# Performance work log

Hardware: AMD Instinct MI355X
Metric: run time of the kernel (lower is better)

## Reference

```python
import jax, jax.numpy as jnp
import numpy as np

# Conv config matching init_kwargs
C_IN, C_OUT = 128, 256
KH, KW = 3, 3
STRIDE = (1, 1)
PADDING = ((1, 1), (1, 1))
DILATION = (1, 1)
B, H, W = 32, 56, 56


def setup_inputs() -> dict:
    key = jax.random.key(0)
    k1, k2, k3 = jax.random.split(key, 3)
    x = jax.random.normal(k1, (B, C_IN, H, W), dtype=jnp.float32)
    # Flattened weight as stored by Conv2DUF: conv.weight.view(O,-1).t() -> [C*kh*kw, O]
    weight = jax.random.normal(k2, (C_IN * KH * KW, C_OUT), dtype=jnp.float32) * 0.02
    bias = jax.random.normal(k3, (C_OUT,), dtype=jnp.float32) * 0.02
    return {"x": x, "weight": weight, "bias": bias}


def reference(x, weight, bias):
    # Conv2DUF computes unfold(x) @ weight + bias, which is exactly a 2D
    # cross-correlation with the original conv kernel. Recover the [O,C,kh,kw]
    # kernel from the flattened [C*kh*kw, O] matrix and use the fused conv
    # primitive (same math, no giant im2col buffer).
    kernel = weight.T.reshape(C_OUT, C_IN, KH, KW)
    out = jax.lax.conv_general_dilated(
        x, kernel,
        window_strides=STRIDE,
        padding=PADDING,
        rhs_dilation=DILATION,
        dimension_numbers=("NCHW", "OIHW", "NCHW"),
    )
    return out + bias[None, :, None, None]
```

## Files before the change

### kernel.cpp

```cpp
#include <hip/hip_runtime.h>
#include <stdint.h>


#define C_INQ 128
#define C_OUTQ 256
#define HDIM 56
#define WDIM 56
#define BDIM 32
#define HP 58
#define WP 58
#define HWPIX (HDIM * WDIM)
#define XT_ELEMS ((size_t)BDIM * HP * WP * C_INQ)
#define XT_BYTES (XT_ELEMS * 2)

typedef __bf16 bf16x8 __attribute__((ext_vector_type(8)));
typedef unsigned short ushort8 __attribute__((ext_vector_type(8)));
typedef float floatx4 __attribute__((ext_vector_type(4)));

__device__ __forceinline__ unsigned short f2bf(float f) {
  union { float f; unsigned int u; } v; v.f = f;
  unsigned int u = v.u;
  unsigned int r = u + 0x7FFFu + ((u >> 16) & 1u);
  return (unsigned short)(r >> 16);
}

__global__ __launch_bounds__(256) void pad_transpose_kernel(
    const float* __restrict__ x, unsigned short* __restrict__ xt) {
  const int blk = blockIdx.x;
  const int b = blk / HP;
  const int hp = blk % HP;
  const int t = threadIdx.x;
  unsigned short* __restrict__ xtrow = xt + (size_t)(b * HP + hp) * (WP * C_INQ);
  if (hp == 0 || hp == HP - 1) {
    for (int i = t; i < WP * C_INQ; i += 256) xtrow[i] = 0;
    return;
  }
  __shared__ float lds[C_INQ * 57];
  const int h = hp - 1;
  const float* __restrict__ xb = x + (size_t)b * C_INQ * HWPIX + h * WDIM;
  for (int i = t; i < C_INQ * WDIM; i += 256) {
    int c = i / WDIM, w = i % WDIM;
    lds[c * 57 + w] = xb[(size_t)c * HWPIX + w];
  }
  __syncthreads();
  for (int i = t; i < WP * C_INQ; i += 256) {
    int wp = i >> 7, c = i & 127;
    float v = (wp == 0 || wp == WP - 1) ? 0.0f : lds[c * 57 + (wp - 1)];
    xtrow[i] = f2bf(v);
  }
}

__global__ __launch_bounds__(256) void weight_transform_kernel(
    const float* __restrict__ w, unsigned short* __restrict__ wt) {
  int idx = blockIdx.x * 256 + threadIdx.x;
  int khw = idx >> 15;
  int r = idx & 32767;
  int n = r >> 7;
  int c = r & 127;
  wt[idx] = f2bf(w[(size_t)(c * 9 + khw) * C_OUTQ + n]);
}

#define BM 128
#define BN 128
#define BK 32

__global__ __launch_bounds__(256, 2) void conv_gemm_kernel(
    const unsigned short* __restrict__ xt,
    const unsigned short* __restrict__ wt,
    const float* __restrict__ bias,
    float* __restrict__ out) {
  __shared__ __align__(16) unsigned short ldsA[BM * BK];
  __shared__ __align__(16) unsigned short ldsB[BN * BK];

  const int t = threadIdx.x;
  const int lane = t & 63;
  const int wave = t >> 6;
  const int tile_m = blockIdx.x;
  const int tile_n = blockIdx.y;
  const int n0 = tile_n * BN;

  size_t baseA[2], baseB[2];
#pragma unroll
  for (int r = 0; r < 2; ++r) {
    int j = r * 256 + t;
    int pix = tile_m * BM + (j >> 2);
    int b = pix / HWPIX;
    int p = pix - b * HWPIX;
    int h = p / WDIM;
    int w = p - h * WDIM;
    baseA[r] = (size_t)((b * HP + h) * WP + w) * C_INQ + (j & 3) * 8;
    baseB[r] = (size_t)(n0 + (j >> 2)) * C_INQ + (j & 3) * 8;
  }
  unsigned short* ldsA_dst[2] = { ldsA + wave * 512, ldsA + 2048 + wave * 512 };
  unsigned short* ldsB_dst[2] = { ldsB + wave * 512, ldsB + 2048 + wave * 512 };

  const int wm = (wave >> 1) * 64;
  const int wn = (wave & 1) * 64;
  const int mrow = lane & 15;
  const int quad = lane >> 4;
  int aoff[4], boff[4];
#pragma unroll
  for (int i = 0; i < 4; ++i) {
    aoff[i] = (wm + i * 16 + mrow) * BK + quad * 8;
    boff[i] = (wn + i * 16 + mrow) * BK + quad * 8;
  }

  floatx4 acc[4][4] = {};

  for (int s = 0; s < 36; ++s) {
    const int khw = s >> 2;
    const int c0 = (s & 3) * 32;
    const int kh = khw / 3;
    const int kw = khw - kh * 3;
    const size_t koffA = (size_t)(kh * WP + kw) * C_INQ + c0;
    const size_t koffB = (size_t)khw * (C_OUTQ * C_INQ) + c0;
#pragma unroll
    for (int r = 0; r < 2; ++r) {
      __builtin_amdgcn_global_load_lds(
          (const __attribute__((address_space(1))) unsigned int*)(xt + baseA[r] + koffA),
          (__attribute__((address_space(3))) unsigned int*)ldsA_dst[r], 16, 0, 0);
      __builtin_amdgcn_global_load_lds(
          (const __attribute__((address_space(1))) unsigned int*)(wt + baseB[r] + koffB),
          (__attribute__((address_space(3))) unsigned int*)ldsB_dst[r], 16, 0, 0);
    }
    __syncthreads();

    bf16x8 afr[4], bfr[4];
#pragma unroll
    for (int i = 0; i < 4; ++i)
      afr[i] = __builtin_bit_cast(bf16x8, *(const ushort8*)(ldsA + aoff[i]));
#pragma unroll
    for (int i = 0; i < 4; ++i)
      bfr[i] = __builtin_bit_cast(bf16x8, *(const ushort8*)(ldsB + boff[i]));
#pragma unroll
    for (int i = 0; i < 4; ++i)
#pragma unroll
      for (int jn = 0; jn < 4; ++jn)
        acc[i][jn] = __builtin_amdgcn_mfma_f32_16x16x32_bf16(afr[i], bfr[jn], acc[i][jn], 0, 0, 0);

    __syncthreads();
  }

#pragma unroll
  for (int jn = 0; jn < 4; ++jn) {
    const int ng = n0 + wn + jn * 16 + mrow;
    const float bv = bias[ng];
#pragma unroll
    for (int i = 0; i < 4; ++i) {
      const int mbase = tile_m * BM + wm + i * 16 + quad * 4;
#pragma unroll
      for (int rg = 0; rg < 4; ++rg) {
        const int mg = mbase + rg;
        const int b = mg / HWPIX;
        const int p = mg - b * HWPIX;
        out[(size_t)b * (C_OUTQ * HWPIX) + (size_t)ng * HWPIX + p] = acc[i][jn][rg] + bv;
      }
    }
  }
}

extern "C" void kernel_launch(void* const* d_in, const int* in_sizes, int n_in,
                              void* d_out, int out_size, void* d_ws, size_t ws_size,
                              hipStream_t stream) {
  const float* x    = (const float*)d_in[0];
  const float* w    = (const float*)d_in[1];
  const float* bias = (const float*)d_in[2];
  float* out = (float*)d_out;

  unsigned short* xt = (unsigned short*)d_ws;
  unsigned short* wt = (unsigned short*)((char*)d_ws + XT_BYTES);

  hipLaunchKernelGGL(pad_transpose_kernel, dim3(BDIM * HP), dim3(256), 0, stream, x, xt);
  hipLaunchKernelGGL(weight_transform_kernel, dim3(1152), dim3(256), 0, stream, w, wt);
  hipLaunchKernelGGL(conv_gemm_kernel, dim3(784, 2), dim3(256), 0, stream, xt, wt, bias, out);
}
```

Baseline: 263.9 us.

## Vectorize pre-transforms, double GEMM K-step with XOR-swizzled LDS, vector stores

The input pad-transpose kernel now reads float4 and writes packed 8-element bf16 vectors. The weight transform now goes through an LDS tile and writes uint4 vectors. The conv GEMM doubles BK to 64, which halves the number of barrier-separated steps, and XOR-swizzles the LDS layout to avoid bank conflicts on fragment reads. The epilogue writes floatx4 along the pixel dimension. Risks are the larger LDS footprint and dropping the min-2-blocks launch bound, both of which may lower occupancy. The floatx4 store also assumes each 4-pixel group never crosses a batch boundary, which holds because HW is divisible by 4.

```diff
diff --git a/kernel.cpp b/kernel.cpp
--- a/kernel.cpp
+++ b/kernel.cpp
@@ -23,6 +23,9 @@
   unsigned int r = u + 0x7FFFu + ((u >> 16) & 1u);
   return (unsigned short)(r >> 16);
 }
+__device__ __forceinline__ unsigned int pack2(float a, float b) {
+  return (unsigned int)f2bf(a) | ((unsigned int)f2bf(b) << 16);
+}
 
 __global__ __launch_bounds__(256) void pad_transpose_kernel(
     const float* __restrict__ x, unsigned short* __restrict__ xt) {
@@ -30,41 +33,72 @@
   const int b = blk / HP;
   const int hp = blk % HP;
   const int t = threadIdx.x;
-  unsigned short* __restrict__ xtrow = xt + (size_t)(b * HP + hp) * (WP * C_INQ);
+  uint4* __restrict__ xtrow4 = (uint4*)(xt + (size_t)(b * HP + hp) * (WP * C_INQ));
   if (hp == 0 || hp == HP - 1) {
-    for (int i = t; i < WP * C_INQ; i += 256) xtrow[i] = 0;
+    for (int i = t; i < 928; i += 256) xtrow4[i] = make_uint4(0, 0, 0, 0);
     return;
   }
-  __shared__ float lds[C_INQ * 57];
+  __shared__ float lds[C_INQ * 62];
   const int h = hp - 1;
-  const float* __restrict__ xb = x + (size_t)b * C_INQ * HWPIX + h * WDIM;
-  for (int i = t; i < C_INQ * WDIM; i += 256) {
-    int c = i / WDIM, w = i % WDIM;
-    lds[c * 57 + w] = xb[(size_t)c * HWPIX + w];
+  const float* __restrict__ xb = x + (size_t)b * C_INQ * HWPIX + (size_t)h * WDIM;
+  for (int i = t; i < 1792; i += 256) {
+    int c = i / 14, w4 = (i - c * 14) * 4;
+    const float4 v = *(const float4*)(xb + (size_t)c * HWPIX + w4);
+    float* d = lds + c * 62 + w4;
+    *(float2*)d = make_float2(v.x, v.y);
+    *(float2*)(d + 2) = make_float2(v.z, v.w);
   }
   __syncthreads();
-  for (int i = t; i < WP * C_INQ; i += 256) {
-    int wp = i >> 7, c = i & 127;
-    float v = (wp == 0 || wp == WP - 1) ? 0.0f : lds[c * 57 + (wp - 1)];
-    xtrow[i] = f2bf(v);
+  for (int j = t; j < 928; j += 256) {
+    int wp = j >> 4, c8 = (j & 15) * 8;
+    uint4 o;
+    if (wp == 0 || wp == WP - 1) {
+      o = make_uint4(0, 0, 0, 0);
+    } else {
+      const float* s = lds + c8 * 62 + (wp - 1);
+      o.x = pack2(s[0],   s[62]);
+      o.y = pack2(s[124], s[186]);
+      o.z = pack2(s[248], s[310]);
+      o.w = pack2(s[372], s[434]);
+    }
+    xtrow4[j] = o;
   }
 }
 
 __global__ __launch_bounds__(256) void weight_transform_kernel(
     const float* __restrict__ w, unsigned short* __restrict__ wt) {
-  int idx = blockIdx.x * 256 + threadIdx.x;
-  int khw = idx >> 15;
-  int r = idx & 32767;
-  int n = r >> 7;
-  int c = r & 127;
-  wt[idx] = f2bf(w[(size_t)(c * 9 + khw) * C_OUTQ + n]);
+  const int bx = blockIdx.x;
+  const int khw = bx >> 4;
+  const int r4 = bx & 15;
+  const int n0w = (r4 >> 2) * 64;
+  const int c32 = (r4 & 3) * 32;
+  const int t = threadIdx.x;
+  __shared__ float lds[32 * 66];
+#pragma unroll
+  for (int r = 0; r < 8; ++r) {
+    int idx = r * 256 + t;
+    int n = idx & 63, c = idx >> 6;
+    lds[c * 66 + n] = w[(size_t)((c32 + c) * 9 + khw) * C_OUTQ + n0w + n];
+  }
+  __syncthreads();
+  {
+    int n = t >> 2, c8 = (t & 3) * 8;
+    const float* s = lds + c8 * 66 + n;
+    uint4 o;
+    o.x = pack2(s[0],   s[66]);
+    o.y = pack2(s[132], s[198]);
+    o.z = pack2(s[264], s[330]);
+    o.w = pack2(s[396], s[462]);
+    *(uint4*)(wt + (size_t)khw * (C_OUTQ * C_INQ) + (size_t)(n0w + n) * C_INQ + c32 + c8) = o;
+  }
 }
 
 #define BM 128
 #define BN 128
-#define BK 32
-
-__global__ __launch_bounds__(256, 2) void conv_gemm_kernel(
+#define BK 64
+#define STEPS 18
+
+__global__ __launch_bounds__(256) void conv_gemm_kernel(
     const unsigned short* __restrict__ xt,
     const unsigned short* __restrict__ wt,
     const float* __restrict__ bias,
@@ -79,82 +113,91 @@
   const int tile_n = blockIdx.y;
   const int n0 = tile_n * BN;
 
-  size_t baseA[2], baseB[2];
-#pragma unroll
-  for (int r = 0; r < 2; ++r) {
-    int j = r * 256 + t;
-    int pix = tile_m * BM + (j >> 2);
+  int gbaseA[4], gbaseB[4];
+#pragma unroll
+  for (int r = 0; r < 4; ++r) {
+    int g = r * 256 + t;
+    int row = g >> 3;
+    int kpart = (g & 7) ^ (row & 7);
+    int pix = tile_m * BM + row;
     int b = pix / HWPIX;
     int p = pix - b * HWPIX;
     int h = p / WDIM;
     int w = p - h * WDIM;
-    baseA[r] = (size_t)((b * HP + h) * WP + w) * C_INQ + (j & 3) * 8;
-    baseB[r] = (size_t)(n0 + (j >> 2)) * C_INQ + (j & 3) * 8;
-  }
-  unsigned short* ldsA_dst[2] = { ldsA + wave * 512, ldsA + 2048 + wave * 512 };
-  unsigned short* ldsB_dst[2] = { ldsB + wave * 512, ldsB + 2048 + wave * 512 };
+    gbaseA[r] = ((b * HP + h) * WP + w) * C_INQ + kpart * 8;
+    gbaseB[r] = (n0 + row) * C_INQ + kpart * 8;
+  }
+  unsigned short* ldsA_dst[4];
+  unsigned short* ldsB_dst[4];
+#pragma unroll
+  for (int r = 0; r < 4; ++r) {
+    ldsA_dst[r] = ldsA + (r * 256 + wave * 64) * 8;
+    ldsB_dst[r] = ldsB + (r * 256 + wave * 64) * 8;
+  }
 
   const int wm = (wave >> 1) * 64;
   const int wn = (wave & 1) * 64;
   const int mrow = lane & 15;
   const int quad = lane >> 4;
-  int aoff[4], boff[4];
-#pragma unroll
-  for (int i = 0; i < 4; ++i) {
-    aoff[i] = (wm + i * 16 + mrow) * BK + quad * 8;
-    boff[i] = (wn + i * 16 + mrow) * BK + quad * 8;
-  }
+  const int xorv = mrow & 7;
 
   floatx4 acc[4][4] = {};
 
-  for (int s = 0; s < 36; ++s) {
-    const int khw = s >> 2;
-    const int c0 = (s & 3) * 32;
+  for (int s = 0; s < STEPS; ++s) {
+    const int khw = s >> 1;
+    const int c0 = (s & 1) * 64;
     const int kh = khw / 3;
     const int kw = khw - kh * 3;
-    const size_t koffA = (size_t)(kh * WP + kw) * C_INQ + c0;
-    const size_t koffB = (size_t)khw * (C_OUTQ * C_INQ) + c0;
-#pragma unroll
-    for (int r = 0; r < 2; ++r) {
+    const int koffA = (kh * WP + kw) * C_INQ + c0;
+    const int koffB = khw * (C_OUTQ * C_INQ) + c0;
+#pragma unroll
+    for (int r = 0; r < 4; ++r) {
       __builtin_amdgcn_global_load_lds(
-          (const __attribute__((address_space(1))) unsigned int*)(xt + baseA[r] + koffA),
+          (const __attribute__((address_space(1))) unsigned int*)(xt + gbaseA[r] + koffA),
           (__attribute__((address_space(3))) unsigned int*)ldsA_dst[r], 16, 0, 0);
       __builtin_amdgcn_global_load_lds(
-          (const __attribute__((address_space(1))) unsigned int*)(wt + baseB[r] + koffB),
+          (const __attribute__((address_space(1))) unsigned int*)(wt + gbaseB[r] + koffB),
           (__attribute__((address_space(3))) unsigned int*)ldsB_dst[r], 16, 0, 0);
     }
     __syncthreads();
 
-    bf16x8 afr[4], bfr[4];
-#pragma unroll
-    for (int i = 0; i < 4; ++i)
-      afr[i] = __builtin_bit_cast(bf16x8, *(const ushort8*)(ldsA + aoff[i]));
-#pragma unroll
-    for (int i = 0; i < 4; ++i)
-      bfr[i] = __builtin_bit_cast(bf16x8, *(const ushort8*)(ldsB + boff[i]));
-#pragma unroll
-    for (int i = 0; i < 4; ++i)
-#pragma unroll
-      for (int jn = 0; jn < 4; ++jn)
-        acc[i][jn] = __builtin_amdgcn_mfma_f32_16x16x32_bf16(afr[i], bfr[jn], acc[i][jn], 0, 0, 0);
-
+#pragma unroll
+    for (int u = 0; u < 2; ++u) {
+      bf16x8 afr[4], bfr[4];
+#pragma unroll
+      for (int i = 0; i < 4; ++i) {
+        int off = (wm + i * 16 + mrow) * 64 + (((u * 4 + quad) ^ xorv) * 8);
+        afr[i] = __builtin_bit_cast(bf16x8, *(const ushort8*)(ldsA + off));
+      }
+#pragma unroll
+      for (int jn = 0; jn < 4; ++jn) {
+        int off = (wn + jn * 16 + mrow) * 64 + (((u * 4 + quad) ^ xorv) * 8);
+        bfr[jn] = __builtin_bit_cast(bf16x8, *(const ushort8*)(ldsB + off));
+      }
+#pragma unroll
+      for (int i = 0; i < 4; ++i)
+#pragma unroll
+        for (int jn = 0; jn < 4; ++jn)
+          acc[i][jn] = __builtin_amdgcn_mfma_f32_16x16x32_bf16(afr[i], bfr[jn], acc[i][jn], 0, 0, 0);
+    }
     __syncthreads();
   }
 
-#pragma unroll
-  for (int jn = 0; jn < 4; ++jn) {
-    const int ng = n0 + wn + jn * 16 + mrow;
-    const float bv = bias[ng];
-#pragma unroll
-    for (int i = 0; i < 4; ++i) {
-      const int mbase = tile_m * BM + wm + i * 16 + quad * 4;
-#pragma unroll
-      for (int rg = 0; rg < 4; ++rg) {
-        const int mg = mbase + rg;
-        const int b = mg / HWPIX;
-        const int p = mg - b * HWPIX;
-        out[(size_t)b * (C_OUTQ * HWPIX) + (size_t)ng * HWPIX + p] = acc[i][jn][rg] + bv;
-      }
+  float bv[4];
+#pragma unroll
+  for (int jn = 0; jn < 4; ++jn) bv[jn] = bias[n0 + wn + jn * 16 + mrow];
+#pragma unroll
+  for (int i = 0; i < 4; ++i) {
+    const int mbase = tile_m * BM + wm + i * 16 + quad * 4;
+    const int b = mbase / HWPIX;
+    const int p = mbase - b * HWPIX;
+    float* obase = out + (size_t)b * (C_OUTQ * HWPIX) + p;
+#pragma unroll
+    for (int jn = 0; jn < 4; ++jn) {
+      const int ng = n0 + wn + jn * 16 + mrow;
+      floatx4 v = acc[i][jn];
+      v[0] += bv[jn]; v[1] += bv[jn]; v[2] += bv[jn]; v[3] += bv[jn];
+      *(floatx4*)(obase + (size_t)ng * HWPIX) = v;
     }
   }
 }
@@ -171,6 +214,6 @@
   unsigned short* wt = (unsigned short*)((char*)d_ws + XT_BYTES);
 
   hipLaunchKernelGGL(pad_transpose_kernel, dim3(BDIM * HP), dim3(256), 0, stream, x, xt);
-  hipLaunchKernelGGL(weight_transform_kernel, dim3(1152), dim3(256), 0, stream, w, wt);
+  hipLaunchKernelGGL(weight_transform_kernel, dim3(144), dim3(256), 0, stream, w, wt);
   hipLaunchKernelGGL(conv_gemm_kernel, dim3(784, 2), dim3(256), 0, stream, xt, wt, bias, out);
 }
```

After: 236.6 us. -10.4%, faster.
